# Performance work log

Measured on AMD Instinct MI355X. Metric: run time of the kernel, lower is better.

The kernel has to match this reference:

```python
import jax, jax.numpy as jnp
import numpy as np

N_NODES = 207
N_EDGES = 1722
N_SLOTS = 288  # 288 / resolution with resolution = 1


def setup_inputs() -> dict:
    key = jax.random.key(0)
    ks = jax.random.split(key, 7)
    B, C, L = 1024, 2, 64
    inputs = jax.random.normal(ks[0], (B, C, N_NODES, L), dtype=jnp.float32)
    weight_diff = jax.random.normal(ks[1], (N_SLOTS, N_EDGES), dtype=jnp.float32) / 1000.0
    bias_diffusion = jax.random.normal(ks[2], (N_SLOTS, N_NODES), dtype=jnp.float32) / 10.0
    weight_self_loop = jax.random.normal(ks[3], (N_SLOTS, N_NODES), dtype=jnp.float32) / 10.0
    ind = jax.random.randint(ks[4], (B,), 0, N_SLOTS, dtype=jnp.int32)
    edge_i = jax.random.randint(ks[5], (N_EDGES,), 0, N_NODES, dtype=jnp.int32)
    edge_j = jax.random.randint(ks[6], (N_EDGES,), 0, N_NODES, dtype=jnp.int32)
    return {"inputs": inputs, "weight_diff": weight_diff,
            "bias_diffusion": bias_diffusion, "weight_self_loop": weight_self_loop,
            "ind": ind, "edge_i": edge_i, "edge_j": edge_j}


def reference(inputs, weight_diff, bias_diffusion, weight_self_loop, ind, edge_i, edge_j):
    # resolution = 1 -> slot index ii == ind
    x = inputs[:, 0, :, :]                      # [B, N, L]
    B, N, _ = x.shape
    w = weight_diff[ind]                        # [B, E] per-sample edge weights
    # symmetric scatter into batched dense adjacency (duplicates sum, as in sparse_coo_tensor)
    A = jnp.zeros((B, N, N), dtype=x.dtype)
    A = A.at[:, edge_i, edge_j].add(w).at[:, edge_j, edge_i].add(w)
    deg = jnp.sum(A, axis=1)                    # [B, N]  (sum over dim 1, as in torch code)
    lap = deg[:, :, None] * jnp.eye(N, dtype=x.dtype) - A  # L = diag(deg) - A
    diffusion = jnp.einsum('nvl,nwv->nwl', x, lap) + bias_diffusion[ind][:, :, None]
    self_loop = weight_self_loop[ind][:, :, None] * x
    return diffusion + x + self_loop
```

## Files before the change

kernel.cpp:

```cpp
#include <hip/hip_runtime.h>

#define N_NODES 207
#define N_EDGES 1722
#define N_SLOTS 288
#define L_DIM   64

__device__ __forceinline__ unsigned int f2bf_rtn_bits_hi(float f) {
    unsigned int u = __float_as_uint(f);
    unsigned int r = u + 0x7FFFu + ((u >> 16) & 1u);
    return r & 0xFFFF0000u;
}

__global__ __launch_bounds__(256) void build_csr_kernel(
    const int* __restrict__ edge_i, const int* __restrict__ edge_j,
    int* __restrict__ row_start, unsigned int* __restrict__ csr_packed) {
    __shared__ int cnt[N_NODES];
    __shared__ int rs[N_NODES + 1];
    const int tid = threadIdx.x;

    for (int n = tid; n < N_NODES; n += 256) cnt[n] = 0;
    __syncthreads();
    for (int e = tid; e < N_EDGES; e += 256) {
        atomicAdd(&cnt[edge_i[e]], 1);
        atomicAdd(&cnt[edge_j[e]], 1);
    }
    __syncthreads();
    if (tid == 0) {
        int acc = 0;
        for (int n = 0; n < N_NODES; ++n) { rs[n] = acc; acc += cnt[n]; }
        rs[N_NODES] = acc;
    }
    __syncthreads();
    for (int n = tid; n <= N_NODES; n += 256) row_start[n] = rs[n];
    for (int n = tid; n < N_NODES; n += 256) cnt[n] = rs[n];
    __syncthreads();
    for (int e = tid; e < N_EDGES; e += 256) {
        const unsigned int i = edge_i[e], j = edge_j[e];
        const unsigned int ep = ((unsigned int)e) << 8;
        int p = atomicAdd(&cnt[i], 1);
        csr_packed[p] = ep | j;
        int q = atomicAdd(&cnt[j], 1);
        csr_packed[q] = ep | i;
    }
}

__global__ __launch_bounds__(256) void coef_kernel(
    const float* __restrict__ weight_diff, const float* __restrict__ bias_diffusion,
    const float* __restrict__ weight_self_loop,
    const int* __restrict__ row_start, const unsigned int* __restrict__ csr_packed,
    float2* __restrict__ coefbias) {
    __shared__ float wrow[N_EDGES];
    const int s = blockIdx.x;
    for (int e = threadIdx.x; e < N_EDGES; e += 256)
        wrow[e] = weight_diff[(size_t)s * N_EDGES + e];
    __syncthreads();
    const int n = threadIdx.x;
    if (n < N_NODES) {
        float d = 0.f;
        const int e0 = row_start[n], e1 = row_start[n + 1];
        for (int k = e0; k < e1; ++k) d += wrow[csr_packed[k] >> 8];
        coefbias[s * N_NODES + n] = make_float2(
            1.f + weight_self_loop[s * N_NODES + n] + d,
            bias_diffusion[s * N_NODES + n]);
    }
}

__global__ __launch_bounds__(512, 8) void diffusion_gcn_kernel(
    const float* __restrict__ inputs,
    const float* __restrict__ weight_diff,
    const int*   __restrict__ ind,
    const int*   __restrict__ row_start,
    const unsigned int* __restrict__ csr_packed,
    const float2* __restrict__ coefbias,
    float* __restrict__ out) {
    __shared__ unsigned short xs[N_NODES * L_DIM];
    __shared__ unsigned int   wnb[2 * N_EDGES];
    __shared__ unsigned short rs[N_NODES + 1];

    const int b    = blockIdx.x;
    const int tid  = threadIdx.x;
    const int slot = ind[b];

    const float* xb = inputs + (size_t)b * (2 * N_NODES * L_DIM);

    const float4* xb4 = (const float4*)xb;
    for (int k = tid; k < (N_NODES * L_DIM) / 4; k += 512) {
        const float4 v = xb4[k];
        const unsigned int lo = (f2bf_rtn_bits_hi(v.x) >> 16) | f2bf_rtn_bits_hi(v.y);
        const unsigned int hi = (f2bf_rtn_bits_hi(v.z) >> 16) | f2bf_rtn_bits_hi(v.w);
        ((uint2*)xs)[k] = make_uint2(lo, hi);
    }
    const float* wrow = weight_diff + (size_t)slot * N_EDGES;
    for (int k = tid; k < 2 * N_EDGES; k += 512) {
        const unsigned int c = csr_packed[k];
        wnb[k] = f2bf_rtn_bits_hi(wrow[c >> 8]) | (c & 255u);
    }
    for (int n = tid; n <= N_NODES; n += 512) rs[n] = (unsigned short)row_start[n];
    __syncthreads();

    const int lane = tid & 63;
    const int wv   = tid >> 6;
    float* ob = out + (size_t)b * (N_NODES * L_DIM);

    for (int n = wv; n < N_NODES; n += 8) {
        const int e0 = rs[n], e1 = rs[n + 1];
        float s = 0.f;
        #pragma unroll 4
        for (int k = e0; k < e1; ++k) {
            const unsigned int p = wnb[k];
            const float w  = __uint_as_float(p & 0xFFFF0000u);
            const float xv = __uint_as_float(
                (unsigned int)xs[(p & 255u) * L_DIM + lane] << 16);
            s = fmaf(w, xv, s);
        }
        const float2 cb = coefbias[slot * N_NODES + n];
        const float  xg = xb[n * L_DIM + lane];
        ob[n * L_DIM + lane] = fmaf(cb.x, xg, cb.y) - s;
    }
}

extern "C" void kernel_launch(void* const* d_in, const int* in_sizes, int n_in,
                              void* d_out, int out_size, void* d_ws, size_t ws_size,
                              hipStream_t stream) {
    const float* inputs           = (const float*)d_in[0];
    const float* weight_diff      = (const float*)d_in[1];
    const float* bias_diffusion   = (const float*)d_in[2];
    const float* weight_self_loop = (const float*)d_in[3];
    const int*   ind              = (const int*)d_in[4];
    const int*   edge_i           = (const int*)d_in[5];
    const int*   edge_j           = (const int*)d_in[6];
    float* out = (float*)d_out;

    const int B = in_sizes[4];

    int*          row_start  = (int*)d_ws;
    unsigned int* csr_packed = (unsigned int*)((char*)d_ws + 832);
    float2*       coefbias   = (float2*)((char*)d_ws + 14608);

    build_csr_kernel<<<1, 256, 0, stream>>>(edge_i, edge_j, row_start, csr_packed);
    coef_kernel<<<N_SLOTS, 256, 0, stream>>>(
        weight_diff, bias_diffusion, weight_self_loop, row_start, csr_packed, coefbias);
    diffusion_gcn_kernel<<<B, 512, 0, stream>>>(
        inputs, weight_diff, ind, row_start, csr_packed, coefbias, out);
}
```

Before: 239.8 us.

## Precompute per-slot edge weight/offset table and keep x in fp32 shared memory

The coefficient kernel now also writes a per-slot table of (fp32 weight, byte offset of neighbour row) pairs in CSR order to workspace. The main kernel reads those pairs straight from global/L2 instead of gathering and packing bf16 weights into shared memory in every block. It also stores x in shared memory as fp32 rather than bf16, which removes the conversion and the precision loss. In exchange each block uses more shared memory (about 53KB), which lowers occupancy, and the edge loop now does global loads. The old path is kept as a fallback when the workspace is too small.

```diff
diff --git a/kernel.cpp b/kernel.cpp
--- a/kernel.cpp
+++ b/kernel.cpp
@@ -1,9 +1,11 @@
 #include <hip/hip_runtime.h>
+#include <stdint.h>
 
 #define N_NODES 207
 #define N_EDGES 1722
 #define N_SLOTS 288
 #define L_DIM   64
+#define NCSR    (2 * N_EDGES)
 
 __device__ __forceinline__ unsigned int f2bf_rtn_bits_hi(float f) {
     unsigned int u = __float_as_uint(f);
@@ -44,16 +46,25 @@
     }
 }
 
-__global__ __launch_bounds__(256) void coef_kernel(
+__global__ __launch_bounds__(256) void coef_eb_kernel(
     const float* __restrict__ weight_diff, const float* __restrict__ bias_diffusion,
     const float* __restrict__ weight_self_loop,
     const int* __restrict__ row_start, const unsigned int* __restrict__ csr_packed,
-    float2* __restrict__ coefbias) {
+    float2* __restrict__ coefbias, uint2* __restrict__ eb) {
     __shared__ float wrow[N_EDGES];
     const int s = blockIdx.x;
     for (int e = threadIdx.x; e < N_EDGES; e += 256)
         wrow[e] = weight_diff[(size_t)s * N_EDGES + e];
     __syncthreads();
+
+    if (eb != nullptr) {
+        uint2* ebs = eb + (size_t)s * NCSR;
+        for (int k = threadIdx.x; k < NCSR; k += 256) {
+            const unsigned int c = csr_packed[k];
+            ebs[k] = make_uint2(__float_as_uint(wrow[c >> 8]), (c & 255u) << 8);
+        }
+    }
+
     const int n = threadIdx.x;
     if (n < N_NODES) {
         float d = 0.f;
@@ -65,7 +76,53 @@
     }
 }
 
-__global__ __launch_bounds__(512, 8) void diffusion_gcn_kernel(
+__global__ __launch_bounds__(512, 6) void diffusion_scalar_kernel(
+    const float* __restrict__ inputs,
+    const int*   __restrict__ ind,
+    const int*   __restrict__ row_start,
+    const uint2* __restrict__ eb,
+    const float2* __restrict__ coefbias,
+    float* __restrict__ out) {
+    __shared__ float xs[N_NODES * L_DIM];
+
+    const int b    = blockIdx.x;
+    const int tid  = threadIdx.x;
+    const int slot = ind[b];
+
+    const float* xb = inputs + (size_t)b * (2 * N_NODES * L_DIM);
+
+    const float4* xb4 = (const float4*)xb;
+    float4* xs4 = (float4*)xs;
+    for (int k = tid; k < (N_NODES * L_DIM) / 4; k += 512) {
+        xs4[k] = xb4[k];
+    }
+    __syncthreads();
+
+    const int lane  = tid & 63;
+    const int lane4 = lane << 2;
+    const int wv    = tid >> 6;
+
+    const uint2*  ebs = eb + (size_t)slot * NCSR;
+    const float2* cbs = coefbias + (size_t)slot * N_NODES;
+    float* ob = out + (size_t)b * (N_NODES * L_DIM);
+    const char* xsb = (const char*)xs;
+
+    for (int n = wv; n < N_NODES; n += 8) {
+        const int e0 = row_start[n], e1 = row_start[n + 1];
+        float s = 0.f;
+        #pragma unroll 4
+        for (int k = e0; k < e1; ++k) {
+            const uint2 p = ebs[k];
+            const float xv = *(const float*)(xsb + (p.y + lane4));
+            s = fmaf(__uint_as_float(p.x), xv, s);
+        }
+        const float2 cb = cbs[n];
+        const float  xg = *(const float*)(xsb + ((n << 8) + lane4));
+        ob[(n << 6) + lane] = fmaf(cb.x, xg, cb.y) - s;
+    }
+}
+
+__global__ __launch_bounds__(512, 8) void diffusion_gcn_fallback(
     const float* __restrict__ inputs,
     const float* __restrict__ weight_diff,
     const int*   __restrict__ ind,
@@ -73,8 +130,8 @@
     const unsigned int* __restrict__ csr_packed,
     const float2* __restrict__ coefbias,
     float* __restrict__ out) {
-    __shared__ unsigned short xs[N_NODES * L_DIM];
-    __shared__ unsigned int   wnb[2 * N_EDGES];
+    __shared__ unsigned short xsh[N_NODES * L_DIM];
+    __shared__ unsigned int   wnb[NCSR];
     __shared__ unsigned short rs[N_NODES + 1];
 
     const int b    = blockIdx.x;
@@ -88,10 +145,10 @@
         const float4 v = xb4[k];
         const unsigned int lo = (f2bf_rtn_bits_hi(v.x) >> 16) | f2bf_rtn_bits_hi(v.y);
         const unsigned int hi = (f2bf_rtn_bits_hi(v.z) >> 16) | f2bf_rtn_bits_hi(v.w);
-        ((uint2*)xs)[k] = make_uint2(lo, hi);
+        ((uint2*)xsh)[k] = make_uint2(lo, hi);
     }
     const float* wrow = weight_diff + (size_t)slot * N_EDGES;
-    for (int k = tid; k < 2 * N_EDGES; k += 512) {
+    for (int k = tid; k < NCSR; k += 512) {
         const unsigned int c = csr_packed[k];
         wnb[k] = f2bf_rtn_bits_hi(wrow[c >> 8]) | (c & 255u);
     }
@@ -110,7 +167,7 @@
             const unsigned int p = wnb[k];
             const float w  = __uint_as_float(p & 0xFFFF0000u);
             const float xv = __uint_as_float(
-                (unsigned int)xs[(p & 255u) * L_DIM + lane] << 16);
+                (unsigned int)xsh[(p & 255u) * L_DIM + lane] << 16);
             s = fmaf(w, xv, s);
         }
         const float2 cb = coefbias[slot * N_NODES + n];
@@ -133,13 +190,24 @@
 
     const int B = in_sizes[4];
 
-    int*          row_start  = (int*)d_ws;
-    unsigned int* csr_packed = (unsigned int*)((char*)d_ws + 832);
-    float2*       coefbias   = (float2*)((char*)d_ws + 14608);
+    char* ws = (char*)d_ws;
+    int*          row_start  = (int*)ws;
+    unsigned int* csr_packed = (unsigned int*)(ws + 832);
+    float2*       coefbias   = (float2*)(ws + 14608);
+    uint2*        eb         = (uint2*)(ws + 491536);
+    const size_t  WS_NEEDED  = 491536 + (size_t)N_SLOTS * NCSR * sizeof(uint2);
+
+    const bool use_eb = (d_ws != nullptr) && (ws_size >= WS_NEEDED);
 
     build_csr_kernel<<<1, 256, 0, stream>>>(edge_i, edge_j, row_start, csr_packed);
-    coef_kernel<<<N_SLOTS, 256, 0, stream>>>(
-        weight_diff, bias_diffusion, weight_self_loop, row_start, csr_packed, coefbias);
-    diffusion_gcn_kernel<<<B, 512, 0, stream>>>(
-        inputs, weight_diff, ind, row_start, csr_packed, coefbias, out);
-}
+    coef_eb_kernel<<<N_SLOTS, 256, 0, stream>>>(
+        weight_diff, bias_diffusion, weight_self_loop, row_start, csr_packed,
+        coefbias, use_eb ? eb : nullptr);
+    if (use_eb) {
+        diffusion_scalar_kernel<<<B, 512, 0, stream>>>(
+            inputs, ind, row_start, eb, coefbias, out);
+    } else {
+        diffusion_gcn_fallback<<<B, 512, 0, stream>>>(
+            inputs, weight_diff, ind, row_start, csr_packed, coefbias, out);
+    }
+}
```

Result: slower. 313.9 us (+30.9%).
